# Kernel optimization log

Measured on AMD Instinct MI355X. Metric: run time of the kernel, lower is better.

## Reference

```python
import jax, jax.numpy as jnp
import numpy as np

TEMPERATURE = 0.5


def setup_inputs() -> dict:
    key = jax.random.key(0)
    k1, k2, k3, k4 = jax.random.split(key, 4)
    B, D = 4096, 256
    return {
        "emb_i": jax.random.normal(k1, (B, D), dtype=jnp.float32),
        "emb_j": jax.random.normal(k2, (B, D), dtype=jnp.float32),
        "tags": jax.random.randint(k3, (B,), 0, 100, dtype=jnp.int32),
        "num_classes": 100,
        "document_ids": jax.random.randint(k4, (B,), 0, 512, dtype=jnp.int32),
    }


def reference(emb_i, emb_j, tags, num_classes, document_ids):
    # L2-normalize rows (cosine similarity of normalized vectors == dot product)
    z_i = emb_i / jnp.linalg.norm(emb_i, axis=1, keepdims=True)
    z_j = emb_j / jnp.linalg.norm(emb_j, axis=1, keepdims=True)
    reps = jnp.concatenate([z_i, z_j], axis=0)          # [2B, D]
    sim = reps @ reps.T                                  # [2B, 2B]
    exp_sim = jnp.exp(sim / TEMPERATURE)                 # [2B, 2B]

    # sum(square(onehot_j - onehot_i))/2 == 1.0 iff labels differ, else 0.0
    tags2 = jnp.concatenate([tags, tags], axis=0)        # [2B]
    docs2 = jnp.concatenate([document_ids, document_ids], axis=0)
    mask = ((tags2[:, None] != tags2[None, :]) & (docs2[:, None] != docs2[None, :])).astype(exp_sim.dtype)

    denom = jnp.sum(mask * exp_sim, axis=1) + 0.1        # [2B]

    B = tags.shape[0]
    idx = jnp.arange(2 * B)
    pair = jnp.concatenate([jnp.arange(B) + B, jnp.arange(B)])  # partner index of each row
    numerator = exp_sim[idx, pair]                       # [2B]

    loss = jnp.sum(-jnp.log(numerator / denom)) / (2 * B)
    return loss
```

## Files before the change

### kernel.cpp

```cpp
#include <hip/hip_runtime.h>
#include <hip/hip_bf16.h>
#include <cstdint>
#include <cstddef>

#define B_ROWS 4096
#define D_DIM  256
#define TWOB   8192
static constexpr float kScale = 2.8853900817779268f;

typedef __bf16 bf16_t;
typedef __bf16 bf16x4 __attribute__((ext_vector_type(4)));
typedef __bf16 bf16x8 __attribute__((ext_vector_type(8)));
typedef float  f32x4  __attribute__((ext_vector_type(4)));

#define WS_Z    0ull
#define WS_KEYS ((size_t)TWOB * D_DIM * 2)
#define WS_DEN  (WS_KEYS + (size_t)TWOB * 4)
#define WS_ACC  (WS_DEN + (size_t)TWOB * 4)


__global__ __launch_bounds__(256) void prep_kernel(
    const float* __restrict__ emb_i, const float* __restrict__ emb_j,
    const int* __restrict__ tags, const int* __restrict__ docs,
    bf16_t* __restrict__ Z, int* __restrict__ keys,
    float* __restrict__ denom, float* __restrict__ accums)
{
  const int t = threadIdx.x;
  const int lane = t & 63, w = t >> 6;
  const int row = blockIdx.x * 4 + w;
  const float* src = (row < B_ROWS) ? (emb_i + (size_t)row * D_DIM)
                                    : (emb_j + (size_t)(row - B_ROWS) * D_DIM);
  float4 v = *(const float4*)(src + lane * 4);
  float ss = v.x * v.x + v.y * v.y + v.z * v.z + v.w * v.w;
  #pragma unroll
  for (int m = 32; m; m >>= 1) ss += __shfl_xor(ss, m, 64);
  float inv = 1.0f / sqrtf(ss);

  bf16x4 q;
  q[0] = (bf16_t)(v.x * inv);
  q[1] = (bf16_t)(v.y * inv);
  q[2] = (bf16_t)(v.z * inv);
  q[3] = (bf16_t)(v.w * inv);

  int chunk = lane >> 4;
  int g     = (lane >> 1) & 7;
  int gs    = g ^ (row & 7);
  int half  = lane & 1;
  *(bf16x4*)(Z + (size_t)row * D_DIM + chunk * 64 + gs * 8 + half * 4) = q;

  if (lane == 0) {
    int rb = (row < B_ROWS) ? row : (row - B_ROWS);
    keys[row] = (tags[rb] << 16) | docs[rb];
    denom[row] = 0.f;
  }
  if (blockIdx.x == 0 && t < 2) accums[t] = 0.f;
}

#define BM 128
#define BK 64
#define NKT (D_DIM / BK)

__global__ __launch_bounds__(256, 2) void fused_kernel(
    const bf16_t* __restrict__ Z, const int* __restrict__ keys,
    float* __restrict__ denom)
{
  __shared__ bf16_t sA[2][BM * BK];
  __shared__ bf16_t sB[2][BM * BK];
  const int tid  = threadIdx.x;
  const int lane = tid & 63;
  const int w    = tid >> 6;
  const int wr = w >> 1, wc = w & 1;
  const int l15 = lane & 15, l4 = lane >> 4;

  int bid = blockIdx.x;
  int rt = (int)((sqrtf(8.0f * (float)bid + 1.0f) - 1.0f) * 0.5f);
  while ((rt + 1) * (rt + 2) / 2 <= bid) ++rt;
  while (rt * (rt + 1) / 2 > bid) --rt;
  const int ct = bid - rt * (rt + 1) / 2;
  const int row0 = rt * BM, col0 = ct * BM;
  const bool offdiag = (rt != ct);

  f32x4 acc[4][4];
  const f32x4 vzero = {0.f, 0.f, 0.f, 0.f};
  #pragma unroll
  for (int mi = 0; mi < 4; ++mi)
    #pragma unroll
    for (int ni = 0; ni < 4; ++ni) acc[mi][ni] = vzero;

  auto STAGE = [&](int buf, int kt) {
    #pragma unroll
    for (int i = 0; i < 4; ++i) {
      int o  = i * 4096 + tid * 16;
      int rl = o >> 7, ob = o & 127;
      const bf16_t* ga = Z + (size_t)(row0 + rl) * D_DIM + kt * 64 + (ob >> 1);
      __builtin_amdgcn_global_load_lds(
          (const __attribute__((address_space(1))) void*)ga,
          (__attribute__((address_space(3))) void*)((char*)&sA[buf][0] + o), 16, 0, 0);
      const bf16_t* gb = Z + (size_t)(col0 + rl) * D_DIM + kt * 64 + (ob >> 1);
      __builtin_amdgcn_global_load_lds(
          (const __attribute__((address_space(1))) void*)gb,
          (__attribute__((address_space(3))) void*)((char*)&sB[buf][0] + o), 16, 0, 0);
    }
  };

  STAGE(0, 0);
  #pragma unroll
  for (int kt = 0; kt < NKT; ++kt) {
    const int buf = kt & 1;
    __syncthreads();
    if (kt < NKT - 1) STAGE(buf ^ 1, kt + 1);

    bf16x8 af[2][4], bfr[2][4];
    #pragma unroll
    for (int h = 0; h < 2; ++h) {
      #pragma unroll
      for (int mi = 0; mi < 4; ++mi) {
        int rl  = wr * 64 + mi * 16 + l15;
        int gsa = (h * 4 + l4) ^ (rl & 7);
        af[h][mi] = *(const bf16x8*)(&sA[buf][rl * 64 + gsa * 8]);
        int cl  = wc * 64 + mi * 16 + l15;
        int gsb = (h * 4 + l4) ^ (cl & 7);
        bfr[h][mi] = *(const bf16x8*)(&sB[buf][cl * 64 + gsb * 8]);
      }
    }
    #pragma unroll
    for (int h = 0; h < 2; ++h)
      #pragma unroll
      for (int mi = 0; mi < 4; ++mi)
        #pragma unroll
        for (int ni = 0; ni < 4; ++ni)
          acc[mi][ni] = __builtin_amdgcn_mfma_f32_16x16x32_bf16(
              af[h][mi], bfr[h][ni], acc[mi][ni], 0, 0, 0);
    __syncthreads();
  }

  int keyr[4][4];
  #pragma unroll
  for (int mi = 0; mi < 4; ++mi)
    #pragma unroll
    for (int j = 0; j < 4; ++j)
      keyr[mi][j] = keys[row0 + wr * 64 + mi * 16 + l4 * 4 + j];
  int keyc[4];
  #pragma unroll
  for (int ni = 0; ni < 4; ++ni)
    keyc[ni] = keys[col0 + wc * 64 + ni * 16 + l15];

  float rowsum[4][4];
  #pragma unroll
  for (int mi = 0; mi < 4; ++mi)
    #pragma unroll
    for (int j = 0; j < 4; ++j) rowsum[mi][j] = 0.f;
  float colsum[4] = {0.f, 0.f, 0.f, 0.f};

  #pragma unroll
  for (int ni = 0; ni < 4; ++ni) {
    #pragma unroll
    for (int mi = 0; mi < 4; ++mi) {
      #pragma unroll
      for (int j = 0; j < 4; ++j) {
        int x = keyr[mi][j] ^ keyc[ni];
        bool m = ((x >> 16) != 0) & ((x & 0xFFFF) != 0);
        float e = m ? __builtin_amdgcn_exp2f(acc[mi][ni][j] * kScale) : 0.f;
        rowsum[mi][j] += e;
        colsum[ni] += e;
      }
    }
  }

  #pragma unroll
  for (int mi = 0; mi < 4; ++mi)
    #pragma unroll
    for (int j = 0; j < 4; ++j) {
      float v = rowsum[mi][j];
      v += __shfl_xor(v, 1, 64);
      v += __shfl_xor(v, 2, 64);
      v += __shfl_xor(v, 4, 64);
      v += __shfl_xor(v, 8, 64);
      if (l15 == 0)
        atomicAdd(&denom[row0 + wr * 64 + mi * 16 + l4 * 4 + j], v);
    }
  if (offdiag) {
    #pragma unroll
    for (int ni = 0; ni < 4; ++ni) {
      float v = colsum[ni];
      v += __shfl_xor(v, 16, 64);
      v += __shfl_xor(v, 32, 64);
      if (l4 == 0)
        atomicAdd(&denom[col0 + wc * 64 + ni * 16 + l15], v);
    }
  }
}

__global__ __launch_bounds__(256) void reduce_kernel(
    const float* __restrict__ denom, const bf16_t* __restrict__ Z,
    float* __restrict__ accums)
{
  const int t = threadIdx.x;
  const int lane = t & 63, w = t >> 6;
  const int g = blockIdx.x * 256 + t;

  float s1 = (g < TWOB) ? __logf(denom[g] + 0.1f) : 0.f;

  float s2 = 0.f;
  int gw = blockIdx.x * 4 + w;
  for (int r = gw; r < B_ROWS; r += 128) {
    bf16x4 a = *(const bf16x4*)(Z + (size_t)r * D_DIM + lane * 4);
    bf16x4 b = *(const bf16x4*)(Z + (size_t)(r + B_ROWS) * D_DIM + lane * 4);
    float d = 0.f;
    #pragma unroll
    for (int i = 0; i < 4; ++i) d = fmaf((float)a[i], (float)b[i], d);
    s2 += d;
  }

  #pragma unroll
  for (int m = 32; m; m >>= 1) {
    s1 += __shfl_xor(s1, m, 64);
    s2 += __shfl_xor(s2, m, 64);
  }
  __shared__ float r1[4], r2[4];
  if (lane == 0) { r1[w] = s1; r2[w] = s2; }
  __syncthreads();
  if (t == 0) {
    atomicAdd(&accums[0], r1[0] + r1[1] + r1[2] + r1[3]);
    atomicAdd(&accums[1], r2[0] + r2[1] + r2[2] + r2[3]);
  }
}

__global__ void finish_kernel(const float* __restrict__ accums, float* __restrict__ out)
{
  if (threadIdx.x == 0)
    out[0] = (accums[0] - 4.0f * accums[1]) * (1.0f / (float)TWOB);
}

extern "C" void kernel_launch(void* const* d_in, const int* in_sizes, int n_in,
                              void* d_out, int out_size, void* d_ws, size_t ws_size,
                              hipStream_t stream) {
  const float* emb_i = (const float*)d_in[0];
  const float* emb_j = (const float*)d_in[1];
  const int*   tags  = (const int*)d_in[2];
  const int*   docs  = (const int*)d_in[4];

  char* ws = (char*)d_ws;
  bf16_t* Z      = (bf16_t*)(ws + WS_Z);
  int*    keys   = (int*)(ws + WS_KEYS);
  float*  denom  = (float*)(ws + WS_DEN);
  float*  accums = (float*)(ws + WS_ACC);
  float*  out    = (float*)d_out;

  prep_kernel<<<TWOB / 4, 256, 0, stream>>>(emb_i, emb_j, tags, docs, Z, keys, denom, accums);
  const int ntiles = (TWOB / BM) * (TWOB / BM + 1) / 2;
  fused_kernel<<<ntiles, 256, 0, stream>>>(Z, keys, denom);
  reduce_kernel<<<TWOB / 256, 256, 0, stream>>>(denom, Z, accums);
  finish_kernel<<<1, 64, 0, stream>>>(accums, out);
}
```

Baseline: 133.7 us.

## Process two tiles per block, compute pair dots in prep, merge tail kernels

```diff
diff --git a/kernel.cpp b/kernel.cpp
--- a/kernel.cpp
+++ b/kernel.cpp
@@ -16,32 +16,33 @@
 #define WS_Z    0ull
 #define WS_KEYS ((size_t)TWOB * D_DIM * 2)
 #define WS_DEN  (WS_KEYS + (size_t)TWOB * 4)
-#define WS_ACC  (WS_DEN + (size_t)TWOB * 4)
+#define WS_PAIR (WS_DEN + (size_t)TWOB * 4)
 
 
 __global__ __launch_bounds__(256) void prep_kernel(
     const float* __restrict__ emb_i, const float* __restrict__ emb_j,
     const int* __restrict__ tags, const int* __restrict__ docs,
     bf16_t* __restrict__ Z, int* __restrict__ keys,
-    float* __restrict__ denom, float* __restrict__ accums)
+    float* __restrict__ denom, float* __restrict__ pair)
 {
+  __shared__ float4 zbuf[4][64];
   const int t = threadIdx.x;
   const int lane = t & 63, w = t >> 6;
-  const int row = blockIdx.x * 4 + w;
-  const float* src = (row < B_ROWS) ? (emb_i + (size_t)row * D_DIM)
-                                    : (emb_j + (size_t)(row - B_ROWS) * D_DIM);
+  const int b = blockIdx.x;
+  const int rlocal = 2 * b + (w & 1);
+  const int row = rlocal + (w >> 1) * B_ROWS;
+  const float* src = (w >> 1) ? (emb_j + (size_t)rlocal * D_DIM)
+                              : (emb_i + (size_t)rlocal * D_DIM);
   float4 v = *(const float4*)(src + lane * 4);
   float ss = v.x * v.x + v.y * v.y + v.z * v.z + v.w * v.w;
   #pragma unroll
   for (int m = 32; m; m >>= 1) ss += __shfl_xor(ss, m, 64);
   float inv = 1.0f / sqrtf(ss);
+  float4 z = {v.x * inv, v.y * inv, v.z * inv, v.w * inv};
+  zbuf[w][lane] = z;
 
   bf16x4 q;
-  q[0] = (bf16_t)(v.x * inv);
-  q[1] = (bf16_t)(v.y * inv);
-  q[2] = (bf16_t)(v.z * inv);
-  q[3] = (bf16_t)(v.w * inv);
-
+  q[0] = (bf16_t)z.x; q[1] = (bf16_t)z.y; q[2] = (bf16_t)z.z; q[3] = (bf16_t)z.w;
   int chunk = lane >> 4;
   int g     = (lane >> 1) & 7;
   int gs    = g ^ (row & 7);
@@ -49,16 +50,23 @@
   *(bf16x4*)(Z + (size_t)row * D_DIM + chunk * 64 + gs * 8 + half * 4) = q;
 
   if (lane == 0) {
-    int rb = (row < B_ROWS) ? row : (row - B_ROWS);
-    keys[row] = (tags[rb] << 16) | docs[rb];
+    keys[row] = (tags[rlocal] << 16) | docs[rlocal];
     denom[row] = 0.f;
   }
-  if (blockIdx.x == 0 && t < 2) accums[t] = 0.f;
+  __syncthreads();
+  if (w < 2) {
+    float4 a = zbuf[w][lane], c = zbuf[w + 2][lane];
+    float d = a.x * c.x + a.y * c.y + a.z * c.z + a.w * c.w;
+    #pragma unroll
+    for (int m = 32; m; m >>= 1) d += __shfl_xor(d, m, 64);
+    if (lane == 0) pair[2 * b + w] = d;
+  }
 }
 
 #define BM 128
 #define BK 64
 #define NKT (D_DIM / BK)
+#define STRIP 2
 
 __global__ __launch_bounds__(256, 2) void fused_kernel(
     const bf16_t* __restrict__ Z, const int* __restrict__ keys,
@@ -72,13 +80,17 @@
   const int wr = w >> 1, wc = w & 1;
   const int l15 = lane & 15, l4 = lane >> 4;
 
-  int bid = blockIdx.x;
-  int rt = (int)((sqrtf(8.0f * (float)bid + 1.0f) - 1.0f) * 0.5f);
-  while ((rt + 1) * (rt + 2) / 2 <= bid) ++rt;
-  while (rt * (rt + 1) / 2 > bid) --rt;
-  const int ct = bid - rt * (rt + 1) / 2;
-  const int row0 = rt * BM, col0 = ct * BM;
-  const bool offdiag = (rt != ct);
+  int t0 = 2 * blockIdx.x;
+  int rt0 = (int)((sqrtf(8.0f * (float)t0 + 1.0f) - 1.0f) * 0.5f);
+  while ((rt0 + 1) * (rt0 + 2) / 2 <= t0) ++rt0;
+  while (rt0 * (rt0 + 1) / 2 > t0) --rt0;
+  int ct0 = t0 - rt0 * (rt0 + 1) / 2;
+  int rt1 = (ct0 < rt0) ? rt0 : rt0 + 1;
+  int ct1 = (ct0 < rt0) ? ct0 + 1 : 0;
+
+  const int  r0s[2] = {rt0 * BM, rt1 * BM};
+  const int  c0s[2] = {ct0 * BM, ct1 * BM};
+  const bool od[2]  = {rt0 != ct0, rt1 != ct1};
 
   f32x4 acc[4][4];
   const f32x4 vzero = {0.f, 0.f, 0.f, 0.f};
@@ -87,28 +99,90 @@
     #pragma unroll
     for (int ni = 0; ni < 4; ++ni) acc[mi][ni] = vzero;
 
-  auto STAGE = [&](int buf, int kt) {
+  auto STAGE = [&](int buf, int ti, int kt) {
     #pragma unroll
     for (int i = 0; i < 4; ++i) {
       int o  = i * 4096 + tid * 16;
       int rl = o >> 7, ob = o & 127;
-      const bf16_t* ga = Z + (size_t)(row0 + rl) * D_DIM + kt * 64 + (ob >> 1);
+      const bf16_t* ga = Z + (size_t)(r0s[ti] + rl) * D_DIM + kt * 64 + (ob >> 1);
       __builtin_amdgcn_global_load_lds(
           (const __attribute__((address_space(1))) void*)ga,
           (__attribute__((address_space(3))) void*)((char*)&sA[buf][0] + o), 16, 0, 0);
-      const bf16_t* gb = Z + (size_t)(col0 + rl) * D_DIM + kt * 64 + (ob >> 1);
+      const bf16_t* gb = Z + (size_t)(c0s[ti] + rl) * D_DIM + kt * 64 + (ob >> 1);
       __builtin_amdgcn_global_load_lds(
           (const __attribute__((address_space(1))) void*)gb,
           (__attribute__((address_space(3))) void*)((char*)&sB[buf][0] + o), 16, 0, 0);
     }
   };
 
-  STAGE(0, 0);
-  #pragma unroll
-  for (int kt = 0; kt < NKT; ++kt) {
-    const int buf = kt & 1;
+  auto EPI = [&](int ti) {
+    const int row0 = r0s[ti], col0 = c0s[ti];
+    int keyr[4][4];
+    #pragma unroll
+    for (int mi = 0; mi < 4; ++mi)
+      #pragma unroll
+      for (int j = 0; j < 4; ++j)
+        keyr[mi][j] = keys[row0 + wr * 64 + mi * 16 + l4 * 4 + j];
+    int keyc[4];
+    #pragma unroll
+    for (int ni = 0; ni < 4; ++ni)
+      keyc[ni] = keys[col0 + wc * 64 + ni * 16 + l15];
+
+    float rowsum[4][4];
+    #pragma unroll
+    for (int mi = 0; mi < 4; ++mi)
+      #pragma unroll
+      for (int j = 0; j < 4; ++j) rowsum[mi][j] = 0.f;
+    float colsum[4] = {0.f, 0.f, 0.f, 0.f};
+
+    #pragma unroll
+    for (int ni = 0; ni < 4; ++ni) {
+      #pragma unroll
+      for (int mi = 0; mi < 4; ++mi) {
+        #pragma unroll
+        for (int j = 0; j < 4; ++j) {
+          int x = keyr[mi][j] ^ keyc[ni];
+          bool m = ((x >> 16) != 0) & ((x & 0xFFFF) != 0);
+          float e = m ? __builtin_amdgcn_exp2f(acc[mi][ni][j] * kScale) : 0.f;
+          rowsum[mi][j] += e;
+          colsum[ni] += e;
+        }
+      }
+    }
+    #pragma unroll
+    for (int mi = 0; mi < 4; ++mi)
+      #pragma unroll
+      for (int j = 0; j < 4; ++j) {
+        float v = rowsum[mi][j];
+        v += __shfl_xor(v, 1, 64);
+        v += __shfl_xor(v, 2, 64);
+        v += __shfl_xor(v, 4, 64);
+        v += __shfl_xor(v, 8, 64);
+        if (l15 == 0)
+          atomicAdd(&denom[row0 + wr * 64 + mi * 16 + l4 * 4 + j], v);
+      }
+    if (od[ti]) {
+      #pragma unroll
+      for (int ni = 0; ni < 4; ++ni) {
+        float v = colsum[ni];
+        v += __shfl_xor(v, 16, 64);
+        v += __shfl_xor(v, 32, 64);
+        if (l4 == 0)
+          atomicAdd(&denom[col0 + wc * 64 + ni * 16 + l15], v);
+      }
+    }
+    #pragma unroll
+    for (int mi = 0; mi < 4; ++mi)
+      #pragma unroll
+      for (int ni = 0; ni < 4; ++ni) acc[mi][ni] = vzero;
+  };
+
+  STAGE(0, 0, 0);
+  #pragma unroll
+  for (int s = 0; s < STRIP * NKT; ++s) {
+    const int buf = s & 1;
     __syncthreads();
-    if (kt < NKT - 1) STAGE(buf ^ 1, kt + 1);
+    if (s < STRIP * NKT - 1) STAGE(buf ^ 1, (s + 1) >> 2, (s + 1) & 3);
 
     bf16x8 af[2][4], bfr[2][4];
     #pragma unroll
@@ -132,104 +206,32 @@
           acc[mi][ni] = __builtin_amdgcn_mfma_f32_16x16x32_bf16(
               af[h][mi], bfr[h][ni], acc[mi][ni], 0, 0, 0);
     __syncthreads();
-  }
-
-  int keyr[4][4];
-  #pragma unroll
-  for (int mi = 0; mi < 4; ++mi)
-    #pragma unroll
-    for (int j = 0; j < 4; ++j)
-      keyr[mi][j] = keys[row0 + wr * 64 + mi * 16 + l4 * 4 + j];
-  int keyc[4];
-  #pragma unroll
-  for (int ni = 0; ni < 4; ++ni)
-    keyc[ni] = keys[col0 + wc * 64 + ni * 16 + l15];
-
-  float rowsum[4][4];
-  #pragma unroll
-  for (int mi = 0; mi < 4; ++mi)
-    #pragma unroll
-    for (int j = 0; j < 4; ++j) rowsum[mi][j] = 0.f;
-  float colsum[4] = {0.f, 0.f, 0.f, 0.f};
-
-  #pragma unroll
-  for (int ni = 0; ni < 4; ++ni) {
-    #pragma unroll
-    for (int mi = 0; mi < 4; ++mi) {
-      #pragma unroll
-      for (int j = 0; j < 4; ++j) {
-        int x = keyr[mi][j] ^ keyc[ni];
-        bool m = ((x >> 16) != 0) & ((x & 0xFFFF) != 0);
-        float e = m ? __builtin_amdgcn_exp2f(acc[mi][ni][j] * kScale) : 0.f;
-        rowsum[mi][j] += e;
-        colsum[ni] += e;
-      }
-    }
-  }
-
-  #pragma unroll
-  for (int mi = 0; mi < 4; ++mi)
-    #pragma unroll
-    for (int j = 0; j < 4; ++j) {
-      float v = rowsum[mi][j];
-      v += __shfl_xor(v, 1, 64);
-      v += __shfl_xor(v, 2, 64);
-      v += __shfl_xor(v, 4, 64);
-      v += __shfl_xor(v, 8, 64);
-      if (l15 == 0)
-        atomicAdd(&denom[row0 + wr * 64 + mi * 16 + l4 * 4 + j], v);
-    }
-  if (offdiag) {
-    #pragma unroll
-    for (int ni = 0; ni < 4; ++ni) {
-      float v = colsum[ni];
-      v += __shfl_xor(v, 16, 64);
-      v += __shfl_xor(v, 32, 64);
-      if (l4 == 0)
-        atomicAdd(&denom[col0 + wc * 64 + ni * 16 + l15], v);
-    }
-  }
-}
-
-__global__ __launch_bounds__(256) void reduce_kernel(
-    const float* __restrict__ denom, const bf16_t* __restrict__ Z,
-    float* __restrict__ accums)
+    if ((s & 3) == 3) EPI(s >> 2);
+  }
+}
+
+__global__ __launch_bounds__(1024) void tail_kernel(
+    const float* __restrict__ denom, const float* __restrict__ pair,
+    float* __restrict__ out)
 {
   const int t = threadIdx.x;
   const int lane = t & 63, w = t >> 6;
-  const int g = blockIdx.x * 256 + t;
-
-  float s1 = (g < TWOB) ? __logf(denom[g] + 0.1f) : 0.f;
-
-  float s2 = 0.f;
-  int gw = blockIdx.x * 4 + w;
-  for (int r = gw; r < B_ROWS; r += 128) {
-    bf16x4 a = *(const bf16x4*)(Z + (size_t)r * D_DIM + lane * 4);
-    bf16x4 b = *(const bf16x4*)(Z + (size_t)(r + B_ROWS) * D_DIM + lane * 4);
-    float d = 0.f;
-    #pragma unroll
-    for (int i = 0; i < 4; ++i) d = fmaf((float)a[i], (float)b[i], d);
-    s2 += d;
-  }
-
-  #pragma unroll
-  for (int m = 32; m; m >>= 1) {
-    s1 += __shfl_xor(s1, m, 64);
-    s2 += __shfl_xor(s2, m, 64);
-  }
-  __shared__ float r1[4], r2[4];
-  if (lane == 0) { r1[w] = s1; r2[w] = s2; }
+  float c = 0.f;
+  #pragma unroll
+  for (int i = 0; i < 8; ++i) c += __logf(denom[t + 1024 * i] + 0.1f);
+  #pragma unroll
+  for (int i = 0; i < 4; ++i) c -= 4.0f * pair[t + 1024 * i];
+  #pragma unroll
+  for (int m = 32; m; m >>= 1) c += __shfl_xor(c, m, 64);
+  __shared__ float red[16];
+  if (lane == 0) red[w] = c;
   __syncthreads();
   if (t == 0) {
-    atomicAdd(&accums[0], r1[0] + r1[1] + r1[2] + r1[3]);
-    atomicAdd(&accums[1], r2[0] + r2[1] + r2[2] + r2[3]);
-  }
-}
-
-__global__ void finish_kernel(const float* __restrict__ accums, float* __restrict__ out)
-{
-  if (threadIdx.x == 0)
-    out[0] = (accums[0] - 4.0f * accums[1]) * (1.0f / (float)TWOB);
+    float s = 0.f;
+    #pragma unroll
+    for (int i = 0; i < 16; ++i) s += red[i];
+    out[0] = s * (1.0f / (float)TWOB);
+  }
 }
 
 extern "C" void kernel_launch(void* const* d_in, const int* in_sizes, int n_in,
@@ -241,15 +243,14 @@
   const int*   docs  = (const int*)d_in[4];
 
   char* ws = (char*)d_ws;
-  bf16_t* Z      = (bf16_t*)(ws + WS_Z);
-  int*    keys   = (int*)(ws + WS_KEYS);
-  float*  denom  = (float*)(ws + WS_DEN);
-  float*  accums = (float*)(ws + WS_ACC);
-  float*  out    = (float*)d_out;
-
-  prep_kernel<<<TWOB / 4, 256, 0, stream>>>(emb_i, emb_j, tags, docs, Z, keys, denom, accums);
+  bf16_t* Z     = (bf16_t*)(ws + WS_Z);
+  int*    keys  = (int*)(ws + WS_KEYS);
+  float*  denom = (float*)(ws + WS_DEN);
+  float*  pair  = (float*)(ws + WS_PAIR);
+  float*  out   = (float*)d_out;
+
+  prep_kernel<<<B_ROWS / 2, 256, 0, stream>>>(emb_i, emb_j, tags, docs, Z, keys, denom, pair);
   const int ntiles = (TWOB / BM) * (TWOB / BM + 1) / 2;
-  fused_kernel<<<ntiles, 256, 0, stream>>>(Z, keys, denom);
-  reduce_kernel<<<TWOB / 256, 256, 0, stream>>>(denom, Z, accums);
-  finish_kernel<<<1, 64, 0, stream>>>(accums, out);
-}
+  fused_kernel<<<ntiles / STRIP, 256, 0, stream>>>(Z, keys, denom);
+  tail_kernel<<<1, 1024, 0, stream>>>(denom, pair, out);
+}
```

After: 122.7 us. 1.09x faster.
